# Kernel optimization log

Hardware: AMD Instinct MI355X
Metric: run time of the kernel (lower is better)

Reference implementation:

```python
import jax, jax.numpy as jnp
import numpy as np

N_NODES = 100000
N_EDGES = 1600000
NFEAT = 128
NHID = 128
NS = 64
NCLASS = 16
B = 8192


def setup_inputs() -> dict:
    key = jax.random.key(0)
    ks = jax.random.split(key, 12)
    s = jax.random.normal(ks[0], (B, NS), dtype=jnp.float32)
    x = jax.random.normal(ks[1], (N_NODES, NFEAT), dtype=jnp.float32)
    row = jax.random.randint(ks[2], (N_EDGES,), 0, N_NODES)
    col = jax.random.randint(ks[3], (N_EDGES,), 0, N_NODES)
    val = jax.random.uniform(ks[4], (N_EDGES,), dtype=jnp.float32)
    index = jax.random.randint(ks[5], (B,), 0, N_NODES)
    # learned parameters (glorot-ish scale)
    W1 = jax.random.normal(ks[6], (NFEAT, NHID), dtype=jnp.float32) / np.sqrt(NFEAT)
    b1 = jnp.zeros((NHID,), dtype=jnp.float32)
    W2 = jax.random.normal(ks[7], (NHID, NHID), dtype=jnp.float32) / np.sqrt(NHID)
    b2 = jnp.zeros((NHID,), dtype=jnp.float32)
    Wl = jax.random.normal(ks[8], (NHID + NS, NCLASS), dtype=jnp.float32) / np.sqrt(NHID + NS)
    bl = jnp.zeros((NCLASS,), dtype=jnp.float32)
    return {"s": s, "x": x, "row": row, "col": col, "val": val,
            "index": index, "W1": W1, "b1": b1, "W2": W2, "b2": b2,
            "Wl": Wl, "bl": bl}


def reference(s, x, row, col, val, index, W1, b1, W2, b2, Wl, bl):
    n = x.shape[0]

    def spmm(h):
        # adj @ h with adj in COO form: out[r] += val_e * h[c]
        return jax.ops.segment_sum(val[:, None] * h[col], row, num_segments=n)

    # dropout is identity in eval mode (training=False)
    h = jax.nn.relu(spmm(x @ W1) + b1)          # gc1 + relu
    h = spmm(h @ W2) + b2                        # gc2
    z = jnp.concatenate([h[index], s], axis=1) @ Wl + bl  # [B, nclass]
    return jax.nn.log_softmax(z, axis=1)
```

## Files before the change

### kernel.cpp

```cpp
#include <hip/hip_runtime.h>
#include <math.h>

#define N_NODES 100000
#define N_EDGES 1600000
#define NFEAT 128
#define NHID 128
#define NS 64
#define NCLASS 16
#define BB 8192

#define B1_SHIFT 11
#define NB1 49
#define SUB_SHIFT 5
#define NSUB 3125
#define CHUNKA 2048
#define HWG 256
#define BINC_CAP 2048

#define NSLICE 8
#define SLICEF 16
#define VSCALE (1.0f / 32767.0f)

typedef unsigned long long ull;
typedef unsigned int uint;


__device__ __forceinline__ unsigned short f2bf(float f) {
  unsigned int u = __float_as_uint(f);
  return (unsigned short)((u + 0x7fffu + ((u >> 16) & 1u)) >> 16);
}
__device__ __forceinline__ float bflo(unsigned int u) {
  return __uint_as_float(u << 16);
}
__device__ __forceinline__ float bfhi(unsigned int u) {
  return __uint_as_float(u & 0xffff0000u);
}
__device__ __forceinline__ unsigned int packbf2(float lo, float hi) {
  return (unsigned int)f2bf(lo) | ((unsigned int)f2bf(hi) << 16);
}


__device__ __forceinline__ ull pack_edge(float v, int r, int c) {
  return ((ull)(__float_as_uint(v) >> 2) << 34) | ((ull)(unsigned)r << 17) | (unsigned)c;
}
__device__ __forceinline__ int edge_col(ull p) { return (int)(p & 0x1FFFFu); }
__device__ __forceinline__ int edge_row(ull p) { return (int)((unsigned)(p >> 17) & 0x1FFFFu); }
__device__ __forceinline__ float edge_val(ull p) {
  return __uint_as_float(((unsigned)(p >> 34)) << 2);
}
__device__ __forceinline__ uint pack4(ull p) {
  uint q = (uint)(edge_val(p) * 32767.f + 0.5f);
  return (uint)edge_col(p) | (q << 17);
}
__device__ __forceinline__ int keep_test(const uint* keep, int r) {
  return (keep[r >> 5] >> (r & 31)) & 1u;
}


__global__ __launch_bounds__(256) void selbuild_kernel(const int* __restrict__ index,
                                                       int* __restrict__ sel,
                                                       uint* __restrict__ keep) {
  int t = blockIdx.x * 256 + threadIdx.x;
  int r = index[t];
  sel[r] = 1;
  atomicOr(&keep[r >> 5], 1u << (r & 31));
}

__global__ __launch_bounds__(256) void selflag_kernel(const int* __restrict__ row,
                                                      const int* __restrict__ col,
                                                      const int* __restrict__ sel,
                                                      uint* __restrict__ keep) {
  int i = blockIdx.x * blockDim.x + threadIdx.x;
  int stride = gridDim.x * blockDim.x;
  for (; i < N_EDGES; i += stride)
    if (sel[row[i]]) {
      int c = col[i];
      atomicOr(&keep[c >> 5], 1u << (c & 31));
    }
}


__global__ __launch_bounds__(256) void histsub_kernel(const int* __restrict__ row,
                                                      const uint* __restrict__ keep,
                                                      int* __restrict__ subcnt) {
  __shared__ int lh[NSUB];
  int tid = threadIdx.x;
  for (int i = tid; i < NSUB; i += 256) lh[i] = 0;
  __syncthreads();
  for (long i = (long)blockIdx.x * 256 + tid; i < N_EDGES; i += (long)HWG * 256) {
    int r = row[i];
    if (keep_test(keep, r)) atomicAdd(&lh[r >> SUB_SHIFT], 1);
  }
  __syncthreads();
  for (int i = tid; i < NSUB; i += 256) {
    int c = lh[i];
    if (c) atomicAdd(&subcnt[i], c);
  }
}


__global__ __launch_bounds__(1024) void scanall_kernel(const int* __restrict__ subcnt,
                                                       int* __restrict__ sub_offs,
                                                       int* __restrict__ gcur1,
                                                       int* __restrict__ gcur2) {
  __shared__ int sd[1024];
  int tid = threadIdx.x;
  int b0 = tid * 4;
  int vv[4];
  int loc = 0;
#pragma unroll
  for (int k = 0; k < 4; ++k) {
    int i = b0 + k;
    vv[k] = (i < NSUB) ? subcnt[i] : 0;
    loc += vv[k];
  }
  sd[tid] = loc;
  __syncthreads();
  for (int o = 1; o < 1024; o <<= 1) {
    int add = (tid >= o) ? sd[tid - o] : 0;
    __syncthreads();
    sd[tid] += add;
    __syncthreads();
  }
  int pre = sd[tid] - loc;
#pragma unroll
  for (int k = 0; k < 4; ++k) {
    int i = b0 + k;
    if (i < NSUB) {
      sub_offs[i] = pre;
      gcur2[i] = pre;
      if ((i & 63) == 0) gcur1[i >> 6] = pre;
      pre += vv[k];
    }
  }
  if (tid == 1023) sub_offs[NSUB] = sd[1023];
}


__global__ __launch_bounds__(256) void binA_kernel(const int* __restrict__ row,
                                                   const int* __restrict__ col,
                                                   const float* __restrict__ val,
                                                   const uint* __restrict__ keep,
                                                   int* __restrict__ gcur1,
                                                   ull* __restrict__ ebuf1) {
  __shared__ ull stage[CHUNKA];
  __shared__ short bkt[CHUNKA];
  __shared__ int hist[NB1], lofs[NB1 + 1], lcur[NB1], gbase[NB1];
  int tid = threadIdx.x;
  for (long base = (long)blockIdx.x * CHUNKA; base < N_EDGES; base += (long)gridDim.x * CHUNKA) {
    int cnt = (int)min((long)CHUNKA, (long)N_EDGES - base);
    if (tid < NB1) hist[tid] = 0;
    __syncthreads();
    ull e[8]; int bk[8];
#pragma unroll
    for (int v = 0; v < 8; ++v) {
      int i = v * 256 + tid;
      bk[v] = -1;
      if (i < cnt) {
        long g = base + i;
        int r = row[g];
        if (keep_test(keep, r)) {
          e[v] = pack_edge(val[g], r, col[g]);
          bk[v] = r >> B1_SHIFT;
          atomicAdd(&hist[bk[v]], 1);
        }
      }
    }
    __syncthreads();
    if (tid < 64) {
      int h = (tid < NB1) ? hist[tid] : 0;
      int x = h;
      for (int o = 1; o < 64; o <<= 1) {
        int y = __shfl_up(x, o);
        if (tid >= o) x += y;
      }
      if (tid < NB1) { lofs[tid] = x - h; lcur[tid] = x - h; }
      if (tid == 63) lofs[NB1] = x;
    }
    __syncthreads();
#pragma unroll
    for (int v = 0; v < 8; ++v) {
      if (bk[v] >= 0) {
        int pos = atomicAdd(&lcur[bk[v]], 1);
        stage[pos] = e[v];
        bkt[pos] = (short)bk[v];
      }
    }
    __syncthreads();
    if (tid < NB1) {
      int h = hist[tid];
      if (h > 0) gbase[tid] = atomicAdd(&gcur1[tid], h);
    }
    __syncthreads();
    int tot = lofs[NB1];
    for (int s = tid; s < tot; s += 256) {
      int lo = bkt[s];
      ebuf1[gbase[lo] + (s - lofs[lo])] = stage[s];
    }
    __syncthreads();
  }
}


__global__ __launch_bounds__(256) void binB_kernel(const ull* __restrict__ ebuf1,
                                                   const int* __restrict__ sub_offs,
                                                   int* __restrict__ gcur2,
                                                   ull* __restrict__ edat8) {
  __shared__ ull stage[CHUNKA];
  __shared__ short bkt[CHUNKA];
  __shared__ int hist[64], lofs[65], lcur[64], gbase[64];
  int tid = threadIdx.x;
  int b1 = blockIdx.x >> 3, w = blockIdx.x & 7;
  int rbeg = sub_offs[b1 << 6];
  int rend = sub_offs[min((b1 + 1) << 6, NSUB)];
  for (int base = rbeg + w * CHUNKA; base < rend; base += 8 * CHUNKA) {
    int cnt = min(CHUNKA, rend - base);
    if (tid < 64) hist[tid] = 0;
    __syncthreads();
    ull e[8]; int bk[8];
#pragma unroll
    for (int v = 0; v < 8; ++v) {
      int i = v * 256 + tid;
      bk[v] = -1;
      if (i < cnt) {
        e[v] = ebuf1[base + i];
        bk[v] = (edge_row(e[v]) >> SUB_SHIFT) - (b1 << 6);
        atomicAdd(&hist[bk[v]], 1);
      }
    }
    __syncthreads();
    if (tid < 64) {
      int h = hist[tid];
      int x = h;
      for (int o = 1; o < 64; o <<= 1) {
        int y = __shfl_up(x, o);
        if (tid >= o) x += y;
      }
      lofs[tid] = x - h;
      lcur[tid] = x - h;
      if (tid == 63) lofs[64] = x;
    }
    __syncthreads();
#pragma unroll
    for (int v = 0; v < 8; ++v) {
      if (bk[v] >= 0) {
        int pos = atomicAdd(&lcur[bk[v]], 1);
        stage[pos] = e[v];
        bkt[pos] = (short)bk[v];
      }
    }
    __syncthreads();
    if (tid < 64) {
      int h = hist[tid];
      if (h > 0) gbase[tid] = atomicAdd(&gcur2[(b1 << 6) + tid], h);
    }
    __syncthreads();
    for (int s = tid; s < cnt; s += 256) {
      int lo = bkt[s];
      edat8[gbase[lo] + (s - lofs[lo])] = stage[s];
    }
    __syncthreads();
  }
}


__global__ __launch_bounds__(256) void binC_kernel(const int* __restrict__ sub_offs,
                                                   const ull* __restrict__ edat8,
                                                   ull* __restrict__ ebuf1,
                                                   uint* __restrict__ edat4,
                                                   int* __restrict__ offs) {
  __shared__ ull es[BINC_CAP];
  __shared__ int rcnt[32], rcur[32];
  int s = blockIdx.x, tid = threadIdx.x;
  int r0 = s << SUB_SHIFT;
  int beg = sub_offs[s], end = sub_offs[s + 1];
  int n = end - beg;
  if (tid < 32) rcnt[tid] = 0;
  __syncthreads();
  if (n <= BINC_CAP) {
    for (int i = tid; i < n; i += 256) {
      ull p = edat8[beg + i];
      es[i] = p;
      atomicAdd(&rcnt[edge_row(p) & 31], 1);
    }
    __syncthreads();
    if (tid < 32) {
      int h = rcnt[tid];
      int x = h;
      for (int o = 1; o < 32; o <<= 1) {
        int y = __shfl_up(x, o, 32);
        if (tid >= o) x += y;
      }
      rcur[tid] = x - h;
      offs[r0 + tid] = beg + x - h;
      if (s == NSUB - 1 && tid == 31) offs[N_NODES] = end;
    }
    __syncthreads();
    for (int i = tid; i < n; i += 256) {
      ull p = es[i];
      int pos = atomicAdd(&rcur[edge_row(p) & 31], 1);
      edat4[beg + pos] = pack4(p);
    }
  } else {
    for (int i = tid; i < n; i += 256) {
      ull p = edat8[beg + i];
      ebuf1[beg + i] = p;
      atomicAdd(&rcnt[edge_row(p) & 31], 1);
    }
    __syncthreads();
    if (tid < 32) {
      int h = rcnt[tid];
      int x = h;
      for (int o = 1; o < 32; o <<= 1) {
        int y = __shfl_up(x, o, 32);
        if (tid >= o) x += y;
      }
      rcur[tid] = x - h;
      offs[r0 + tid] = beg + x - h;
      if (s == NSUB - 1 && tid == 31) offs[N_NODES] = end;
    }
    __syncthreads();
    for (int i = tid; i < n; i += 256) {
      ull p = ebuf1[beg + i];
      int pos = atomicAdd(&rcur[edge_row(p) & 31], 1);
      edat4[beg + pos] = pack4(p);
    }
  }
}


typedef __attribute__((ext_vector_type(8))) __bf16 bf16x8;
typedef __attribute__((ext_vector_type(4))) float f32x4;
union FragU { uint4 u; bf16x8 b; };

#define LDSTR 68

__global__ __launch_bounds__(256) void gemm1_kernel(const float* __restrict__ A,
                                                    const float* __restrict__ W,
                                                    unsigned short* __restrict__ C,
                                                    int nrows) {
  __shared__ uint As_s[64 * LDSTR];
  __shared__ uint Wt_s[128 * LDSTR];
  int tid = threadIdx.x;
  int rbase = blockIdx.x * 64;

  {
    int n = tid & 127, hh = tid >> 7;
#pragma unroll
    for (int kk = 0; kk < 32; ++kk) {
      int kc = hh * 32 + kk;
      Wt_s[n * LDSTR + kc] = packbf2(W[(2 * kc) * 128 + n], W[(2 * kc + 1) * 128 + n]);
    }
  }
  {
    const float4* src = (const float4*)(A + (long)rbase * 128);
#pragma unroll
    for (int i = 0; i < 8; ++i) {
      int f = i * 256 + tid;
      int m = f >> 5;
      float4 v = (rbase + m < nrows) ? src[f] : make_float4(0.f, 0.f, 0.f, 0.f);
      int c = (f & 31) * 2;
      As_s[m * LDSTR + c]     = packbf2(v.x, v.y);
      As_s[m * LDSTR + c + 1] = packbf2(v.z, v.w);
    }
  }
  __syncthreads();

  int w = tid >> 6, lane = tid & 63;
  int quad = lane >> 4, lr = lane & 15;
  int n0 = w * 32;

  f32x4 acc[4][2];
#pragma unroll
  for (int mt = 0; mt < 4; ++mt)
#pragma unroll
    for (int nt = 0; nt < 2; ++nt) acc[mt][nt] = (f32x4){0.f, 0.f, 0.f, 0.f};

#pragma unroll
  for (int kk = 0; kk < 4; ++kk) {
    int kc = kk * 16 + quad * 4;
    FragU fb0, fb1;
    fb0.u = *(const uint4*)&Wt_s[(n0 + lr) * LDSTR + kc];
    fb1.u = *(const uint4*)&Wt_s[(n0 + 16 + lr) * LDSTR + kc];
#pragma unroll
    for (int mt = 0; mt < 4; ++mt) {
      FragU fa;
      fa.u = *(const uint4*)&As_s[(mt * 16 + lr) * LDSTR + kc];
      acc[mt][0] = __builtin_amdgcn_mfma_f32_16x16x32_bf16(fa.b, fb0.b, acc[mt][0], 0, 0, 0);
      acc[mt][1] = __builtin_amdgcn_mfma_f32_16x16x32_bf16(fa.b, fb1.b, acc[mt][1], 0, 0, 0);
    }
  }

#pragma unroll
  for (int mt = 0; mt < 4; ++mt) {
#pragma unroll
    for (int nt = 0; nt < 2; ++nt) {
      unsigned short* cs = C + (size_t)(w * 2 + nt) * (N_NODES * SLICEF);
#pragma unroll
      for (int r = 0; r < 4; ++r) {
        int row = rbase + mt * 16 + quad * 4 + r;
        if (row < nrows) cs[(size_t)row * SLICEF + lr] = f2bf(acc[mt][nt][r]);
      }
    }
  }
}


__global__ __launch_bounds__(256) void gemm2f_kernel(const float* __restrict__ g2,
                                                     const float* __restrict__ W2,
                                                     const float* __restrict__ b2,
                                                     const float* __restrict__ s_in,
                                                     const float* __restrict__ Wl,
                                                     const float* __restrict__ bl,
                                                     float* __restrict__ out) {
  __shared__ uint smem[13056];
  uint* Wt_s = smem;
  uint* As_s = smem + 128 * LDSTR;
  float* ts  = (float*)smem;
  float* Wls = (float*)(smem + 128 * LDSTR);
  int tid = threadIdx.x;
  int rbase = blockIdx.x * 64;

  {
    int n = tid & 127, hh = tid >> 7;
#pragma unroll
    for (int kk = 0; kk < 32; ++kk) {
      int kc = hh * 32 + kk;
      Wt_s[n * LDSTR + kc] = packbf2(W2[(2 * kc) * 128 + n], W2[(2 * kc + 1) * 128 + n]);
    }
  }
  {
    const float4* src = (const float4*)(g2 + (long)rbase * 128);
#pragma unroll
    for (int i = 0; i < 8; ++i) {
      int f = i * 256 + tid;
      int m = f >> 5, c = (f & 31) * 2;
      float4 v = src[f];
      As_s[m * LDSTR + c]     = packbf2(v.x, v.y);
      As_s[m * LDSTR + c + 1] = packbf2(v.z, v.w);
    }
  }
  __syncthreads();

  int w = tid >> 6, lane = tid & 63;
  int quad = lane >> 4, lr = lane & 15;
  int n0 = w * 32;

  f32x4 acc[4][2];
#pragma unroll
  for (int mt = 0; mt < 4; ++mt)
#pragma unroll
    for (int nt = 0; nt < 2; ++nt) acc[mt][nt] = (f32x4){0.f, 0.f, 0.f, 0.f};

#pragma unroll
  for (int kk = 0; kk < 4; ++kk) {
    int kc = kk * 16 + quad * 4;
    FragU fb0, fb1;
    fb0.u = *(const uint4*)&Wt_s[(n0 + lr) * LDSTR + kc];
    fb1.u = *(const uint4*)&Wt_s[(n0 + 16 + lr) * LDSTR + kc];
#pragma unroll
    for (int mt = 0; mt < 4; ++mt) {
      FragU fa;
      fa.u = *(const uint4*)&As_s[(mt * 16 + lr) * LDSTR + kc];
      acc[mt][0] = __builtin_amdgcn_mfma_f32_16x16x32_bf16(fa.b, fb0.b, acc[mt][0], 0, 0, 0);
      acc[mt][1] = __builtin_amdgcn_mfma_f32_16x16x32_bf16(fa.b, fb1.b, acc[mt][1], 0, 0, 0);
    }
  }
  __syncthreads();

#pragma unroll
  for (int mt = 0; mt < 4; ++mt) {
#pragma unroll
    for (int nt = 0; nt < 2; ++nt) {
      int col = n0 + nt * 16 + lr;
      float bv = b2[col];
#pragma unroll
      for (int r = 0; r < 4; ++r)
        ts[(mt * 16 + quad * 4 + r) * 129 + col] = acc[mt][nt][r] + bv;
    }
  }
  for (int i = tid; i < 192 * 16; i += 256) Wls[i] = Wl[i];
  __syncthreads();

  int q = lane & 3;
  int mrow = w * 16 + (lane >> 2);
  int b = rbase + mrow;
  float z[16];
#pragma unroll
  for (int c = 0; c < 16; ++c) z[c] = 0.f;
  int k0 = q * 48;
  for (int kk = 0; kk < 48; ++kk) {
    int k = k0 + kk;
    float xv = (k < 128) ? ts[mrow * 129 + k] : s_in[(long)b * 64 + (k - 128)];
    const float* wp = Wls + k * 16;
#pragma unroll
    for (int c = 0; c < 16; ++c) z[c] = fmaf(xv, wp[c], z[c]);
  }
#pragma unroll
  for (int c = 0; c < 16; ++c) {
    z[c] += __shfl_xor(z[c], 1);
    z[c] += __shfl_xor(z[c], 2);
  }
  if (q == 0) {
#pragma unroll
    for (int c = 0; c < 16; ++c) z[c] += bl[c];
    float mx = z[0];
#pragma unroll
    for (int c = 1; c < 16; ++c) mx = fmaxf(mx, z[c]);
    float sum = 0.f;
#pragma unroll
    for (int c = 0; c < 16; ++c) sum += expf(z[c] - mx);
    float lse = mx + logf(sum);
    float4* ob = (float4*)(out + (long)b * 16);
    ob[0] = make_float4(z[0] - lse, z[1] - lse, z[2] - lse, z[3] - lse);
    ob[1] = make_float4(z[4] - lse, z[5] - lse, z[6] - lse, z[7] - lse);
    ob[2] = make_float4(z[8] - lse, z[9] - lse, z[10] - lse, z[11] - lse);
    ob[3] = make_float4(z[12] - lse, z[13] - lse, z[14] - lse, z[15] - lse);
  }
}


__device__ __forceinline__ void fma_row(float* acc, float v, uint4 u) {
  acc[0] = fmaf(v, bflo(u.x), acc[0]);
  acc[1] = fmaf(v, bfhi(u.x), acc[1]);
  acc[2] = fmaf(v, bflo(u.y), acc[2]);
  acc[3] = fmaf(v, bfhi(u.y), acc[3]);
  acc[4] = fmaf(v, bflo(u.z), acc[4]);
  acc[5] = fmaf(v, bfhi(u.z), acc[5]);
  acc[6] = fmaf(v, bflo(u.w), acc[6]);
  acc[7] = fmaf(v, bfhi(u.w), acc[7]);
}

__global__ __launch_bounds__(256) void spmm_row_kernel(const int* __restrict__ offs,
                                                       const uint* __restrict__ edat4,
                                                       const unsigned short* __restrict__ a,
                                                       const float* __restrict__ bias,
                                                       unsigned short* __restrict__ h1,
                                                       const uint* __restrict__ keep) {
  int s = blockIdx.x & 7;
  int rblk = blockIdx.x >> 3;
  int tid = threadIdx.x, lane = tid & 63;
  int r = rblk * 16 + (tid >> 4);
  int g = (lane >> 1) & 7, h = lane & 1, h8 = h * 8;
  if (!keep_test(keep, r)) return;
  const unsigned short* as = a + (size_t)s * (N_NODES * SLICEF);
  int j = offs[r] + g, jend = offs[r + 1];
  float acc[8] = {0.f, 0.f, 0.f, 0.f, 0.f, 0.f, 0.f, 0.f};
  for (; j + 8 < jend; j += 16) {
    uint e0 = edat4[j];
    uint e1 = edat4[j + 8];
    uint4 u0 = *(const uint4*)(as + (size_t)(e0 & 0x1FFFFu) * SLICEF + h8);
    uint4 u1 = *(const uint4*)(as + (size_t)(e1 & 0x1FFFFu) * SLICEF + h8);
    fma_row(acc, (float)(e0 >> 17) * VSCALE, u0);
    fma_row(acc, (float)(e1 >> 17) * VSCALE, u1);
  }
  if (j < jend) {
    uint e = edat4[j];
    uint4 u = *(const uint4*)(as + (size_t)(e & 0x1FFFFu) * SLICEF + h8);
    fma_row(acc, (float)(e >> 17) * VSCALE, u);
  }
#pragma unroll
  for (int k = 0; k < 8; ++k) {
    acc[k] += __shfl_xor(acc[k], 2);
    acc[k] += __shfl_xor(acc[k], 4);
    acc[k] += __shfl_xor(acc[k], 8);
  }
  if ((lane & 14) == 0) {
    const float* bp = bias + s * SLICEF + h8;
    float4 b0 = *(const float4*)bp;
    float4 b1v = *(const float4*)(bp + 4);
    uint4 o;
    o.x = packbf2(fmaxf(acc[0] + b0.x, 0.f), fmaxf(acc[1] + b0.y, 0.f));
    o.y = packbf2(fmaxf(acc[2] + b0.z, 0.f), fmaxf(acc[3] + b0.w, 0.f));
    o.z = packbf2(fmaxf(acc[4] + b1v.x, 0.f), fmaxf(acc[5] + b1v.y, 0.f));
    o.w = packbf2(fmaxf(acc[6] + b1v.z, 0.f), fmaxf(acc[7] + b1v.w, 0.f));
    *(uint4*)(h1 + (size_t)s * (N_NODES * SLICEF) + (size_t)r * SLICEF + h8) = o;
  }
}

__global__ __launch_bounds__(256) void spmm_sel_kernel(const int* __restrict__ offs,
                                                       const uint* __restrict__ edat4,
                                                       const unsigned short* __restrict__ h1,
                                                       const int* __restrict__ index,
                                                       float* __restrict__ g2) {
  int s = blockIdx.x & 7;
  int bblk = blockIdx.x >> 3;
  int tid = threadIdx.x, lane = tid & 63;
  int b = bblk * 16 + (tid >> 4);
  int g = (lane >> 1) & 7, h = lane & 1, h8 = h * 8;
  const unsigned short* hs = h1 + (size_t)s * (N_NODES * SLICEF);
  int r = index[b];
  int j = offs[r] + g, jend = offs[r + 1];
  float acc[8] = {0.f, 0.f, 0.f, 0.f, 0.f, 0.f, 0.f, 0.f};
  for (; j + 8 < jend; j += 16) {
    uint e0 = edat4[j];
    uint e1 = edat4[j + 8];
    uint4 u0 = *(const uint4*)(hs + (size_t)(e0 & 0x1FFFFu) * SLICEF + h8);
    uint4 u1 = *(const uint4*)(hs + (size_t)(e1 & 0x1FFFFu) * SLICEF + h8);
    fma_row(acc, (float)(e0 >> 17) * VSCALE, u0);
    fma_row(acc, (float)(e1 >> 17) * VSCALE, u1);
  }
  if (j < jend) {
    uint e = edat4[j];
    uint4 u = *(const uint4*)(hs + (size_t)(e & 0x1FFFFu) * SLICEF + h8);
    fma_row(acc, (float)(e >> 17) * VSCALE, u);
  }
#pragma unroll
  for (int k = 0; k < 8; ++k) {
    acc[k] += __shfl_xor(acc[k], 2);
    acc[k] += __shfl_xor(acc[k], 4);
    acc[k] += __shfl_xor(acc[k], 8);
  }
  if ((lane & 14) == 0) {
    float* op = g2 + (size_t)b * 128 + s * SLICEF + h8;
    *(float4*)op = make_float4(acc[0], acc[1], acc[2], acc[3]);
    *(float4*)(op + 4) = make_float4(acc[4], acc[5], acc[6], acc[7]);
  }
}


extern "C" void kernel_launch(void* const* d_in, const int* in_sizes, int n_in,
                              void* d_out, int out_size, void* d_ws, size_t ws_size,
                              hipStream_t stream) {
  const float* s_in  = (const float*)d_in[0];
  const float* x     = (const float*)d_in[1];
  const int*   row   = (const int*)d_in[2];
  const int*   col   = (const int*)d_in[3];
  const float* val   = (const float*)d_in[4];
  const int*   index = (const int*)d_in[5];
  const float* W1    = (const float*)d_in[6];
  const float* b1    = (const float*)d_in[7];
  const float* W2    = (const float*)d_in[8];
  const float* b2    = (const float*)d_in[9];
  const float* Wl    = (const float*)d_in[10];
  const float* bl    = (const float*)d_in[11];
  float* out = (float*)d_out;

  ull* edat8 = (ull*)d_ws;
  ull* ebuf1 = edat8 + N_EDGES;
  uint* edat4 = (uint*)ebuf1;
  unsigned short* a  = (unsigned short*)(ebuf1 + N_EDGES);
  unsigned short* h1 = a + (size_t)N_NODES * 128;
  float* g2   = (float*)(h1 + (size_t)N_NODES * 128);
  int* sel    = (int*)(g2 + (size_t)BB * 128);
  int* subcnt = sel + N_NODES;
  uint* keep  = (uint*)(subcnt + NSUB);
  int* offs   = (int*)(keep + NSUB);
  int* sub_offs = offs + (N_NODES + 1);
  int* gcur1  = sub_offs + (NSUB + 1);
  int* gcur2  = gcur1 + NB1;

  hipMemsetAsync(sel, 0, (N_NODES + 2 * NSUB) * sizeof(int), stream);

  selbuild_kernel<<<BB / 256, 256, 0, stream>>>(index, sel, keep);
  selflag_kernel<<<4096, 256, 0, stream>>>(row, col, sel, keep);
  histsub_kernel<<<HWG, 256, 0, stream>>>(row, keep, subcnt);
  scanall_kernel<<<1, 1024, 0, stream>>>(subcnt, sub_offs, gcur1, gcur2);

  binA_kernel<<<512, 256, 0, stream>>>(row, col, val, keep, gcur1, ebuf1);
  binB_kernel<<<NB1 * 8, 256, 0, stream>>>(ebuf1, sub_offs, gcur2, edat8);
  binC_kernel<<<NSUB, 256, 0, stream>>>(sub_offs, edat8, ebuf1, edat4, offs);

  gemm1_kernel<<<(N_NODES + 63) / 64, 256, 0, stream>>>(x, W1, a, N_NODES);
  spmm_row_kernel<<<(N_NODES / 16) * NSLICE, 256, 0, stream>>>(offs, edat4, a, b1, h1, keep);
  spmm_sel_kernel<<<(BB / 16) * NSLICE, 256, 0, stream>>>(offs, edat4, h1, index, g2);
  gemm2f_kernel<<<BB / 64, 256, 0, stream>>>(g2, W2, b2, s_in, Wl, bl, out);
}
```

Baseline: 332.9 us.

## Use fp16 packed math in SpMM and compact kept rows into a list

Switches the gemm1 output and both SpMM kernels from bf16 storage with fp32 accumulation to fp16 storage with packed half2 FMA accumulation. The row SpMM is also driven by a compacted list of kept rows built by a new rowlist kernel, so blocks no longer exit early on masked rows. Each row now uses 8 lanes instead of 16. The aim is fewer ALU instructions and less wasted wavefront occupancy. The cost is fp16 accumulation over ~16 edges per row, which loses precision and risks overflow, plus an extra kernel and memset.

```diff
diff --git a/kernel.cpp b/kernel.cpp
--- a/kernel.cpp
+++ b/kernel.cpp
@@ -1,4 +1,5 @@
 #include <hip/hip_runtime.h>
+#include <hip/hip_fp16.h>
 #include <math.h>
 
 #define N_NODES 100000
@@ -29,14 +30,28 @@
   unsigned int u = __float_as_uint(f);
   return (unsigned short)((u + 0x7fffu + ((u >> 16) & 1u)) >> 16);
 }
-__device__ __forceinline__ float bflo(unsigned int u) {
-  return __uint_as_float(u << 16);
-}
-__device__ __forceinline__ float bfhi(unsigned int u) {
-  return __uint_as_float(u & 0xffff0000u);
-}
 __device__ __forceinline__ unsigned int packbf2(float lo, float hi) {
   return (unsigned int)f2bf(lo) | ((unsigned int)f2bf(hi) << 16);
+}
+
+
+__device__ __forceinline__ __half2 h2zero() {
+  return __builtin_bit_cast(__half2, 0u);
+}
+__device__ __forceinline__ __half2 h2shfl_add(__half2 a, int m) {
+  int t = __shfl_xor(__builtin_bit_cast(int, a), m);
+  return __hadd2(a, __builtin_bit_cast(__half2, t));
+}
+__device__ __forceinline__ uint relu2(uint u) {
+  uint mm = ((u >> 15) & 0x10001u) * 0xFFFFu;
+  return u & ~mm;
+}
+union U4H { uint4 u4; __half2 h[4]; };
+
+__device__ __forceinline__ void fma_row_h(__half2* acc, __half2 v, uint4 u) {
+  U4H q; q.u4 = u;
+#pragma unroll
+  for (int k = 0; k < 4; ++k) acc[k] = __hfma2(v, q.h[k], acc[k]);
 }
 
 
@@ -77,6 +92,24 @@
       int c = col[i];
       atomicOr(&keep[c >> 5], 1u << (c & 31));
     }
+}
+
+
+__global__ __launch_bounds__(256) void rowlist_kernel(const uint* __restrict__ keep,
+                                                      int* __restrict__ rowlist,
+                                                      int* __restrict__ nkept) {
+  int w = blockIdx.x * 256 + threadIdx.x;
+  if (w >= NSUB) return;
+  uint b = keep[w];
+  int c = __popc(b);
+  if (!c) return;
+  int base = atomicAdd(nkept, c);
+  int r0 = w << 5;
+  while (b) {
+    int i = __ffs(b) - 1;
+    rowlist[base++] = r0 + i;
+    b &= b - 1;
+  }
 }
 
 
@@ -395,11 +428,11 @@
   for (int mt = 0; mt < 4; ++mt) {
 #pragma unroll
     for (int nt = 0; nt < 2; ++nt) {
-      unsigned short* cs = C + (size_t)(w * 2 + nt) * (N_NODES * SLICEF);
+      __half* cs = (__half*)(C + (size_t)(w * 2 + nt) * (N_NODES * SLICEF));
 #pragma unroll
       for (int r = 0; r < 4; ++r) {
         int row = rbase + mt * 16 + quad * 4 + r;
-        if (row < nrows) cs[(size_t)row * SLICEF + lr] = f2bf(acc[mt][nt][r]);
+        if (row < nrows) cs[(size_t)row * SLICEF + lr] = __float2half(acc[mt][nt][r]);
       }
     }
   }
@@ -520,60 +553,56 @@
 }
 
 
-__device__ __forceinline__ void fma_row(float* acc, float v, uint4 u) {
-  acc[0] = fmaf(v, bflo(u.x), acc[0]);
-  acc[1] = fmaf(v, bfhi(u.x), acc[1]);
-  acc[2] = fmaf(v, bflo(u.y), acc[2]);
-  acc[3] = fmaf(v, bfhi(u.y), acc[3]);
-  acc[4] = fmaf(v, bflo(u.z), acc[4]);
-  acc[5] = fmaf(v, bfhi(u.z), acc[5]);
-  acc[6] = fmaf(v, bflo(u.w), acc[6]);
-  acc[7] = fmaf(v, bfhi(u.w), acc[7]);
-}
-
 __global__ __launch_bounds__(256) void spmm_row_kernel(const int* __restrict__ offs,
                                                        const uint* __restrict__ edat4,
                                                        const unsigned short* __restrict__ a,
                                                        const float* __restrict__ bias,
                                                        unsigned short* __restrict__ h1,
-                                                       const uint* __restrict__ keep) {
+                                                       const int* __restrict__ rowlist,
+                                                       const int* __restrict__ nkept) {
+  int nk = *nkept;
+  int rblk = blockIdx.x >> 3;
+  if (rblk * 32 >= nk) return;
   int s = blockIdx.x & 7;
-  int rblk = blockIdx.x >> 3;
   int tid = threadIdx.x, lane = tid & 63;
-  int r = rblk * 16 + (tid >> 4);
-  int g = (lane >> 1) & 7, h = lane & 1, h8 = h * 8;
-  if (!keep_test(keep, r)) return;
+  int li = rblk * 32 + (tid >> 3);
+  int g = (lane >> 1) & 3, h = lane & 1, h8 = h * 8;
   const unsigned short* as = a + (size_t)s * (N_NODES * SLICEF);
-  int j = offs[r] + g, jend = offs[r + 1];
-  float acc[8] = {0.f, 0.f, 0.f, 0.f, 0.f, 0.f, 0.f, 0.f};
-  for (; j + 8 < jend; j += 16) {
+  bool active = li < nk;
+  int r = 0, j = 0, jend = 0;
+  if (active) {
+    r = rowlist[li];
+    j = offs[r] + g;
+    jend = offs[r + 1];
+  }
+  __half2 acc[4] = {h2zero(), h2zero(), h2zero(), h2zero()};
+  for (; j + 4 < jend; j += 8) {
     uint e0 = edat4[j];
-    uint e1 = edat4[j + 8];
+    uint e1 = edat4[j + 4];
     uint4 u0 = *(const uint4*)(as + (size_t)(e0 & 0x1FFFFu) * SLICEF + h8);
     uint4 u1 = *(const uint4*)(as + (size_t)(e1 & 0x1FFFFu) * SLICEF + h8);
-    fma_row(acc, (float)(e0 >> 17) * VSCALE, u0);
-    fma_row(acc, (float)(e1 >> 17) * VSCALE, u1);
+    fma_row_h(acc, __float2half2_rn((float)(e0 >> 17) * VSCALE), u0);
+    fma_row_h(acc, __float2half2_rn((float)(e1 >> 17) * VSCALE), u1);
   }
   if (j < jend) {
     uint e = edat4[j];
     uint4 u = *(const uint4*)(as + (size_t)(e & 0x1FFFFu) * SLICEF + h8);
-    fma_row(acc, (float)(e >> 17) * VSCALE, u);
-  }
-#pragma unroll
-  for (int k = 0; k < 8; ++k) {
-    acc[k] += __shfl_xor(acc[k], 2);
-    acc[k] += __shfl_xor(acc[k], 4);
-    acc[k] += __shfl_xor(acc[k], 8);
-  }
-  if ((lane & 14) == 0) {
+    fma_row_h(acc, __float2half2_rn((float)(e >> 17) * VSCALE), u);
+  }
+#pragma unroll
+  for (int k = 0; k < 4; ++k) {
+    acc[k] = h2shfl_add(acc[k], 2);
+    acc[k] = h2shfl_add(acc[k], 4);
+  }
+  if (active && (lane & 6) == 0) {
     const float* bp = bias + s * SLICEF + h8;
     float4 b0 = *(const float4*)bp;
     float4 b1v = *(const float4*)(bp + 4);
     uint4 o;
-    o.x = packbf2(fmaxf(acc[0] + b0.x, 0.f), fmaxf(acc[1] + b0.y, 0.f));
-    o.y = packbf2(fmaxf(acc[2] + b0.z, 0.f), fmaxf(acc[3] + b0.w, 0.f));
-    o.z = packbf2(fmaxf(acc[4] + b1v.x, 0.f), fmaxf(acc[5] + b1v.y, 0.f));
-    o.w = packbf2(fmaxf(acc[6] + b1v.z, 0.f), fmaxf(acc[7] + b1v.w, 0.f));
+    o.x = relu2(__builtin_bit_cast(uint, __hadd2(acc[0], __floats2half2_rn(b0.x, b0.y))));
+    o.y = relu2(__builtin_bit_cast(uint, __hadd2(acc[1], __floats2half2_rn(b0.z, b0.w))));
+    o.z = relu2(__builtin_bit_cast(uint, __hadd2(acc[2], __floats2half2_rn(b1v.x, b1v.y))));
+    o.w = relu2(__builtin_bit_cast(uint, __hadd2(acc[3], __floats2half2_rn(b1v.z, b1v.w))));
     *(uint4*)(h1 + (size_t)s * (N_NODES * SLICEF) + (size_t)r * SLICEF + h8) = o;
   }
 }
@@ -586,35 +615,36 @@
   int s = blockIdx.x & 7;
   int bblk = blockIdx.x >> 3;
   int tid = threadIdx.x, lane = tid & 63;
-  int b = bblk * 16 + (tid >> 4);
-  int g = (lane >> 1) & 7, h = lane & 1, h8 = h * 8;
+  int b = bblk * 32 + (tid >> 3);
+  int g = (lane >> 1) & 3, h = lane & 1, h8 = h * 8;
   const unsigned short* hs = h1 + (size_t)s * (N_NODES * SLICEF);
   int r = index[b];
   int j = offs[r] + g, jend = offs[r + 1];
-  float acc[8] = {0.f, 0.f, 0.f, 0.f, 0.f, 0.f, 0.f, 0.f};
-  for (; j + 8 < jend; j += 16) {
+  __half2 acc[4] = {h2zero(), h2zero(), h2zero(), h2zero()};
+  for (; j + 4 < jend; j += 8) {
     uint e0 = edat4[j];
-    uint e1 = edat4[j + 8];
+    uint e1 = edat4[j + 4];
     uint4 u0 = *(const uint4*)(hs + (size_t)(e0 & 0x1FFFFu) * SLICEF + h8);
     uint4 u1 = *(const uint4*)(hs + (size_t)(e1 & 0x1FFFFu) * SLICEF + h8);
-    fma_row(acc, (float)(e0 >> 17) * VSCALE, u0);
-    fma_row(acc, (float)(e1 >> 17) * VSCALE, u1);
+    fma_row_h(acc, __float2half2_rn((float)(e0 >> 17) * VSCALE), u0);
+    fma_row_h(acc, __float2half2_rn((float)(e1 >> 17) * VSCALE), u1);
   }
   if (j < jend) {
     uint e = edat4[j];
     uint4 u = *(const uint4*)(hs + (size_t)(e & 0x1FFFFu) * SLICEF + h8);
-    fma_row(acc, (float)(e >> 17) * VSCALE, u);
-  }
-#pragma unroll
-  for (int k = 0; k < 8; ++k) {
-    acc[k] += __shfl_xor(acc[k], 2);
-    acc[k] += __shfl_xor(acc[k], 4);
-    acc[k] += __shfl_xor(acc[k], 8);
-  }
-  if ((lane & 14) == 0) {
+    fma_row_h(acc, __float2half2_rn((float)(e >> 17) * VSCALE), u);
+  }
+#pragma unroll
+  for (int k = 0; k < 4; ++k) {
+    acc[k] = h2shfl_add(acc[k], 2);
+    acc[k] = h2shfl_add(acc[k], 4);
+  }
+  if ((lane & 6) == 0) {
     float* op = g2 + (size_t)b * 128 + s * SLICEF + h8;
-    *(float4*)op = make_float4(acc[0], acc[1], acc[2], acc[3]);
-    *(float4*)(op + 4) = make_float4(acc[4], acc[5], acc[6], acc[7]);
+    *(float4*)op = make_float4(__low2float(acc[0]), __high2float(acc[0]),
+                               __low2float(acc[1]), __high2float(acc[1]));
+    *(float4*)(op + 4) = make_float4(__low2float(acc[2]), __high2float(acc[2]),
+                                     __low2float(acc[3]), __high2float(acc[3]));
   }
 }
 
@@ -643,26 +673,30 @@
   unsigned short* h1 = a + (size_t)N_NODES * 128;
   float* g2   = (float*)(h1 + (size_t)N_NODES * 128);
   int* sel    = (int*)(g2 + (size_t)BB * 128);
+  int* rowlist = sel;
   int* subcnt = sel + N_NODES;
   uint* keep  = (uint*)(subcnt + NSUB);
   int* offs   = (int*)(keep + NSUB);
   int* sub_offs = offs + (N_NODES + 1);
   int* gcur1  = sub_offs + (NSUB + 1);
   int* gcur2  = gcur1 + NB1;
+  int* nkept  = gcur2 + NSUB;
 
   hipMemsetAsync(sel, 0, (N_NODES + 2 * NSUB) * sizeof(int), stream);
+  hipMemsetAsync(nkept, 0, sizeof(int), stream);
 
   selbuild_kernel<<<BB / 256, 256, 0, stream>>>(index, sel, keep);
   selflag_kernel<<<4096, 256, 0, stream>>>(row, col, sel, keep);
   histsub_kernel<<<HWG, 256, 0, stream>>>(row, keep, subcnt);
   scanall_kernel<<<1, 1024, 0, stream>>>(subcnt, sub_offs, gcur1, gcur2);
+  rowlist_kernel<<<(NSUB + 255) / 256, 256, 0, stream>>>(keep, rowlist, nkept);
 
   binA_kernel<<<512, 256, 0, stream>>>(row, col, val, keep, gcur1, ebuf1);
   binB_kernel<<<NB1 * 8, 256, 0, stream>>>(ebuf1, sub_offs, gcur2, edat8);
   binC_kernel<<<NSUB, 256, 0, stream>>>(sub_offs, edat8, ebuf1, edat4, offs);
 
   gemm1_kernel<<<(N_NODES + 63) / 64, 256, 0, stream>>>(x, W1, a, N_NODES);
-  spmm_row_kernel<<<(N_NODES / 16) * NSLICE, 256, 0, stream>>>(offs, edat4, a, b1, h1, keep);
-  spmm_sel_kernel<<<(BB / 16) * NSLICE, 256, 0, stream>>>(offs, edat4, h1, index, g2);
+  spmm_row_kernel<<<NSUB * NSLICE, 256, 0, stream>>>(offs, edat4, a, b1, h1, rowlist, nkept);
+  spmm_sel_kernel<<<(BB / 32) * NSLICE, 256, 0, stream>>>(offs, edat4, h1, index, g2);
   gemm2f_kernel<<<BB / 64, 256, 0, stream>>>(g2, W2, b2, s_in, Wl, bl, out);
 }
```

Result: faster. 316.2 us (-5.0%).
